# Optimization experiments

Hardware: AMD Instinct MI355X
Metric: run time of the kernel (lower is better)

The kernel has to match this reference:

```python
import jax, jax.numpy as jnp
import numpy as np

N_WAY = 5
K_SHOT = 1
PROJ_DIM = 64
TEMPERATURE = 0.2
EPS_COS = 1e-12   # F.normalize eps in InnerproductSimilarity (cosine)
EPS_L2 = 1e-16    # _l2norm eps


def setup_inputs() -> dict:
    key = jax.random.key(0)
    ks = jax.random.split(key, 8)
    b, q, u, c, h, w = 2, 15, 20, 64, 21, 21
    s = N_WAY * K_SHOT
    std = float(np.sqrt(2.0 / PROJ_DIM))  # kaiming init used for 1x1 conv heads
    return {
        "support_xf": jax.random.normal(ks[0], (b, s, c, h, w), jnp.float32),
        "support_y": jax.random.randint(ks[1], (b, s), 0, N_WAY),
        "query_xf": jax.random.normal(ks[2], (b, q, c, h, w), jnp.float32),
        "query_y": jax.random.randint(ks[3], (b, q), 0, N_WAY),
        "unlabeled_xf": jax.random.normal(ks[4], (b, u, c, h, w), jnp.float32),
        "key_w": jax.random.normal(ks[5], (PROJ_DIM, c), jnp.float32) * std,
        "query_w": jax.random.normal(ks[6], (PROJ_DIM, c), jnp.float32) * std,
        "value_w": jax.random.normal(ks[7], (PROJ_DIM, c), jnp.float32) * std,
    }


def _dual_nn_selection(support_xf, unlabeled_xf):
    """Mutual-NN (dual NN) selection of unlabeled positions per class.
    Returns padded gather indices idx [b,n_way,L], 0/1 validity sel [b,n_way,L], and L.
    L is data-dependent (max per-(batch,class) count), computed eagerly like the
    original torch code's umask_length."""
    b, u, c, h, w = unlabeled_xf.shape
    M_u, M_s = u * h * w, K_SHOT * h * w
    unl = jnp.transpose(unlabeled_xf, (0, 2, 1, 3, 4)).reshape(b, c, M_u)  # [b,c,M_u]
    sup = jnp.transpose(support_xf.reshape(b, N_WAY, K_SHOT, c, h, w), (0, 1, 3, 2, 4, 5)).reshape(b, N_WAY, c, M_s)
    # cosine InnerproductSimilarity: normalize over channel dim
    sup_n = sup / jnp.maximum(jnp.linalg.norm(sup, axis=2, keepdims=True), EPS_COS)
    unl_n = unl / jnp.maximum(jnp.linalg.norm(unl, axis=1, keepdims=True), EPS_COS)
    u2s = jnp.einsum('bcm,bncs->bnms', unl_n, sup_n)  # [b,n_way,M_u,M_s]
    flat = jnp.transpose(u2s, (0, 2, 1, 3)).reshape(b, M_u, N_WAY * M_s)
    s_near = jnp.argmax(flat, axis=1)   # [b, n_way*M_s] nearest unlabeled pos per support slot
    u_near = jnp.argmax(flat, axis=2)   # [b, M_u] nearest support slot per unlabeled pos
    mutual = (jnp.take_along_axis(s_near, u_near, axis=1) == jnp.arange(M_u)[None, :])  # [b,M_u]
    cls = jnp.argmax(jnp.max(u2s, axis=-1), axis=1)  # [b,M_u] class assignment
    umask = jnp.transpose(jax.nn.one_hot(cls, N_WAY, dtype=jnp.float32), (0, 2, 1)) \
            * mutual[:, None, :].astype(jnp.float32)  # [b,n_way,M_u]
    L = int(jnp.max(jnp.sum(umask, axis=-1)))  # umask_length (data-dependent)
    order = jnp.argsort(-umask, axis=-1)       # stable: selected positions first, original order
    idx = order[:, :, :L]                      # [b,n_way,L]
    sel = jnp.take_along_axis(umask, idx, axis=-1)  # 1 = real feature, 0 = zero padding
    return idx, sel, L


def _forward_core(support_xf, query_xf, unlabeled_xf, key_w, query_w, value_w, query_y, idx, sel):
    b, q, c, h, w = query_xf.shape
    hw = h * w
    u = unlabeled_xf.shape[1]
    M_u, M_s = u * hw, K_SHOT * hw
    unl = jnp.transpose(unlabeled_xf, (0, 2, 1, 3, 4)).reshape(b, c, M_u)
    sup = jnp.transpose(support_xf.reshape(b, N_WAY, K_SHOT, c, h, w), (0, 1, 3, 2, 4, 5)).reshape(b, N_WAY, c, M_s)
    # ragged per-class scatter realized as padded gather (zeros where sel==0)
    gathered = jnp.take_along_axis(unl[:, None, :, :], idx[:, :, None, :], axis=-1)  # [b,n_way,c,L]
    unl_dual = gathered * sel[:, :, None, :]
    s_cat_u = jnp.concatenate([sup, unl_dual], axis=-1)  # [b,n_way,c,M_s+L]
    # 1x1 conv heads == channel matmuls
    qf = query_xf.reshape(b, q, c, hw)
    q_proj = jnp.einsum('oc,bqcm->bqom', query_w, qf)   # [b,q,64,hw]
    v_query = jnp.einsum('oc,bqcm->bqom', value_w, qf)  # [b,q,64,hw]
    k_sup = jnp.einsum('oc,bncl->bnol', key_w, s_cat_u)
    v_sup = jnp.einsum('oc,bncl->bnol', value_w, s_cat_u)
    simi = jnp.einsum('bqom,bnol->bqnml', q_proj, k_sup) / np.float32(np.sqrt(PROJ_DIM))  # [b,q,n,hw,Ms+L]
    Lt = simi.shape[-1]
    # _MNN with compensate_for_single == False (encoder == 'FourLayer_64F')
    merged = jnp.transpose(simi, (0, 1, 3, 2, 4)).reshape(b, q, hw, N_WAY * Lt)
    q_near = jnp.argmax(merged, axis=-1)  # [b,q,hw]
    s_near = jnp.argmax(merged, axis=-2)  # [b,q,n_way*Lt]
    q_mask = (jnp.take_along_axis(s_near, q_near, axis=-1) == jnp.arange(hw)[None, None, :]).astype(simi.dtype)
    att = jax.nn.softmax(simi * q_mask[:, :, None, :, None], axis=-1)
    aligned = jnp.einsum('bqnml,bnol->bqnmo', att, v_sup)  # [b,q,n_way,hw,64]
    aligned = aligned / (jnp.linalg.norm(aligned, axis=-1, keepdims=True) + EPS_L2)
    vq = v_query / (jnp.linalg.norm(v_query, axis=2, keepdims=True) + EPS_L2)
    simi2 = (jnp.einsum('bqnmo,bqok->bqnmk', aligned, vq) + 1.0) * 0.5  # FourLayer_64F rescale
    logits = jnp.sum(jnp.max(simi2, axis=-2), axis=-1).reshape(b * q, N_WAY)  # topk(1,-2)+mean == max
    logp = jax.nn.log_softmax(logits / np.float32(TEMPERATURE), axis=-1)
    y = query_y.reshape(b * q)
    return -jnp.mean(jnp.take_along_axis(logp, y[:, None], axis=1))  # CrossEntropyLoss


def reference(support_xf, support_y, query_xf, query_y, unlabeled_xf, key_w, query_w, value_w):
    idx, sel, _ = _dual_nn_selection(support_xf, unlabeled_xf)
    return _forward_core(support_xf, query_xf, unlabeled_xf, key_w, query_w, value_w, query_y, idx, sel)
```

## Files before the change

kernel.cpp:

```cpp
#include <hip/hip_runtime.h>
#include <math.h>

#define B 2
#define Q 15
#define U 20
#define C 64
#define HW 441
#define NW 5
#define MU (U*HW)
#define MS HW
#define NJ (NW*MS)
#define PD 64
#define LCAP NJ
#define LTCAP 896
#define SCAP 896
#define MSP 448
#define MUP 8832
#define NJP 2304
#define NEGF (-3.402823466e38f)

__device__ unsigned long long g_snearpack[B*NJ];
__device__ unsigned long long g_unearpack[B*MU];
__device__ int   g_counts[B*NW];
__device__ int   g_L[1];
__device__ int   g_selidx[B*NW*LCAP];
__device__ float g_unln[(size_t)B*C*MUP];
__device__ float g_supn[(size_t)B*C*NJP];
__device__ float g_ksup[(size_t)B*NW*PD*LTCAP];
__device__ float g_vsup[(size_t)B*NW*PD*LTCAP];
__device__ float g_vsupT[(size_t)B*NW*LTCAP*PD];
__device__ float g_vbarn[B*NW*PD];
__device__ float g_qproj[(size_t)B*Q*PD*MSP];
__device__ float g_vqn[(size_t)B*Q*PD*MSP];
__device__ unsigned long long g_rowpack[(size_t)B*Q*NW*MSP];
__device__ unsigned long long g_snear2pack[(size_t)B*Q*NW*LTCAP];
__device__ int   g_qmrows[B*Q*MSP];
__device__ int   g_qmcount[B*Q];
__device__ unsigned g_cmax[(size_t)B*Q*NW*MSP];
__device__ float g_logits[B*Q*NW];
__device__ float g_scores[(size_t)B*Q*NW*MSP*SCAP];

__device__ __forceinline__ unsigned enc_f(float f){
  unsigned b=__float_as_uint(f);
  return (b&0x80000000u)? ~b : (b|0x80000000u);
}
__device__ __forceinline__ float dec_f(unsigned k){
  unsigned b=(k&0x80000000u)?(k^0x80000000u):~k;
  return __uint_as_float(b);
}
__device__ __forceinline__ unsigned long long pk_make(float v,int idx){
  return ((unsigned long long)enc_f(v)<<32)|(unsigned)~(unsigned)idx;
}
__device__ __forceinline__ int pk_idx(unsigned long long p){
  return (int)~(unsigned)(p&0xFFFFFFFFull);
}

__global__ void k_init(){
  int i=blockIdx.x*256+threadIdx.x;
  if (i<B*NJ) g_snearpack[i]=0ull;
  if (i<B*MU) g_unearpack[i]=0ull;
  if (i<B*Q*NW*MSP){ g_rowpack[i]=0ull; g_cmax[i]=0u; }
  if (i<B*Q*NW*LTCAP) g_snear2pack[i]=0ull;
  if (i<B*C*(MUP-MU)){
    int b=i/(C*(MUP-MU)), r=i%(C*(MUP-MU)), c=r/(MUP-MU), m=MU+r%(MUP-MU);
    g_unln[((size_t)b*C+c)*MUP+m]=0.f;
  }
  if (i<B*C*(NJP-NJ)){
    int b=i/(C*(NJP-NJ)), r=i%(C*(NJP-NJ)), c=r/(NJP-NJ), j=NJ+r%(NJP-NJ);
    g_supn[((size_t)b*C+c)*NJP+j]=0.f;
  }
  if (i==0) g_L[0]=0;
}

__global__ void k_norms(const float* __restrict__ sup, const float* __restrict__ unl){
  int i=blockIdx.x*256+threadIdx.x;
  if (i<B*MU){
    int b=i/MU, m=i%MU, ui=m/HW, p=m%HW;
    const float* base=unl+((size_t)(b*U+ui)*C)*HW+p;
    float ss=0.f;
    for (int c=0;c<C;c++){ float x=base[(size_t)c*HW]; ss+=x*x; }
    float rn=1.f/fmaxf(sqrtf(ss),1e-12f);
    for (int c=0;c<C;c++) g_unln[((size_t)b*C+c)*MUP+m]=base[(size_t)c*HW]*rn;
  }
  if (i<B*NJ){
    int b=i/NJ, j=i%NJ, n=j/MS, s=j%MS;
    const float* base=sup+((size_t)(b*NW+n)*C)*HW+s;
    float ss=0.f;
    for (int c=0;c<C;c++){ float x=base[(size_t)c*HW]; ss+=x*x; }
    float rn=1.f/fmaxf(sqrtf(ss),1e-12f);
    for (int c=0;c<C;c++) g_supn[((size_t)b*C+c)*NJP+j]=base[(size_t)c*HW]*rn;
  }
}

__global__ __launch_bounds__(256) void k_u2s(){
  int blk=blockIdx.x;
  int jc=blk%18; blk/=18;
  int rb=blk%69; int b=blk/69;
  int m0=rb*128, j0=jc*128;
  int mv=min(128,MU-m0);
  int jv=min(128,NJ-j0);
  int tid=threadIdx.x, tm=tid>>4, tl=tid&15;
  int lane=tid&63, w=tid>>6;
  __shared__ __align__(16) float Ut[32*128];
  __shared__ __align__(16) float Pt[32*128];
  __shared__ unsigned long long colred[512];
  const size_t ub=(size_t)b*C*MUP+m0;
  const size_t pb=(size_t)b*C*NJP+j0;
  float s[8][8]={};
  #pragma unroll
  for (int h=0;h<2;h++){
    __syncthreads();
    for (int k4=tid;k4<1024;k4+=256){
      int c=k4>>5, mq=k4&31;
      *(float4*)&Ut[c*128+mq*4]=*(const float4*)&g_unln[ub+(size_t)(h*32+c)*MUP+mq*4];
      *(float4*)&Pt[c*128+mq*4]=*(const float4*)&g_supn[pb+(size_t)(h*32+c)*NJP+mq*4];
    }
    __syncthreads();
    for (int c=0;c<32;c++){
      float a[8],b0[4],b1[4];
      *(float4*)&a[0]=*(const float4*)&Ut[c*128+tm*8];
      *(float4*)&a[4]=*(const float4*)&Ut[c*128+tm*8+4];
      *(float4*)b0=*(const float4*)&Pt[c*128+tl*4];
      *(float4*)b1=*(const float4*)&Pt[c*128+64+tl*4];
      #pragma unroll
      for (int i=0;i<8;i++)
        #pragma unroll
        for (int j=0;j<4;j++){ s[i][j]=fmaf(a[i],b0[j],s[i][j]); s[i][j+4]=fmaf(a[i],b1[j],s[i][j+4]); }
    }
  }
  #pragma unroll
  for (int i=0;i<8;i++){
    int mm=tm*8+i;
    unsigned long long p=0ull;
    if (mm<mv){
      #pragma unroll
      for (int j=0;j<8;j++){
        int jj=(j<4)?(tl*4+j):(64+tl*4+(j-4));
        if (jj<jv){
          unsigned long long c2=pk_make(s[i][j],j0+jj);
          if (c2>p) p=c2;
        }
      }
    }
    #pragma unroll
    for (int mk=1;mk<16;mk<<=1){ unsigned long long o=__shfl_xor(p,mk); if (o>p) p=o; }
    if (tl==0 && mm<mv && p) atomicMax(&g_unearpack[b*MU+m0+mm],p);
  }
  #pragma unroll
  for (int j=0;j<8;j++){
    int jj=(j<4)?(tl*4+j):(64+tl*4+(j-4));
    unsigned long long p=0ull;
    #pragma unroll
    for (int i=0;i<8;i++){
      int mm=tm*8+i;
      if (mm<mv){
        unsigned long long c2=pk_make(s[i][j],m0+mm);
        if (c2>p) p=c2;
      }
    }
    {
      unsigned long long o=__shfl_xor(p,16); if (o>p) p=o;
      o=__shfl_xor(p,32); if (o>p) p=o;
    }
    if ((lane>>4)==0) colred[w*128+jj]=p;
  }
  __syncthreads();
  if (tid<128 && tid<jv){
    unsigned long long p=colred[tid];
    if (colred[128+tid]>p) p=colred[128+tid];
    if (colred[256+tid]>p) p=colred[256+tid];
    if (colred[384+tid]>p) p=colred[384+tid];
    if (p) atomicMax(&g_snearpack[b*NJ+j0+tid],p);
  }
}

__global__ __launch_bounds__(256) void k_compact(){
  int b=blockIdx.x/NW, n=blockIdx.x%NW;
  int tid=threadIdx.x, lane=tid&63, w=tid>>6;
  __shared__ int wtot[4];
  int base=0;
  for (int m0=0;m0<MU;m0+=256){
    int m=m0+tid;
    bool flag=false;
    if (m<MU){
      int j=pk_idx(g_unearpack[b*MU+m]);
      flag=(j/MS==n) && (pk_idx(g_snearpack[b*NJ+j])==m);
    }
    unsigned long long bal=__ballot(flag);
    if (lane==0) wtot[w]=(int)__popcll(bal);
    __syncthreads();
    int wpre=0, tot=0;
    #pragma unroll
    for (int ww=0;ww<4;ww++){ if (ww<w) wpre+=wtot[ww]; tot+=wtot[ww]; }
    if (flag){
      int pre=(int)__popcll(bal&((1ull<<lane)-1ull));
      g_selidx[(b*NW+n)*LCAP+base+wpre+pre]=m;
    }
    base+=tot;
    __syncthreads();
  }
  if (tid==0){ g_counts[b*NW+n]=base; atomicMax(&g_L[0],base); }
}

__global__ __launch_bounds__(256) void k_kv(const float* __restrict__ sup, const float* __restrict__ unl,
                                            const float* __restrict__ kw, const float* __restrict__ vw){
  int blk=blockIdx.x;
  int lb=blk%(LTCAP/64); blk/=(LTCAP/64);
  int n=blk%NW, b=blk/NW;
  int Lt=MS+g_L[0];
  if (lb*64>=Lt) return;
  int cnt=g_counts[b*NW+n];
  int tid=threadIdx.x, lane=tid&63, w=tid>>6;
  __shared__ float F[4096];
  __shared__ const float* ptr_s[64];
  if (tid<64){
    int l=lb*64+tid;
    const float* p=nullptr;
    if (l<MS) p=&sup[((size_t)(b*NW+n)*C)*HW+l];
    else if (l<MS+cnt){
      int mg=g_selidx[(b*NW+n)*LCAP+(l-MS)];
      int ui=mg/HW, pp=mg%HW;
      p=&unl[((size_t)(b*U+ui)*C)*HW+pp];
    }
    ptr_s[tid]=p;
  }
  __syncthreads();
  for (int k=tid;k<4096;k+=256){
    int c=k>>6, ll=k&63;
    const float* p=ptr_s[ll];
    F[c*64+ll]=p?p[(size_t)c*HW]:0.f;
  }
  __syncthreads();
  int l=lb*64+lane;
  size_t ob=((size_t)(b*NW+n)*PD)*LTCAP+l;
  size_t tb=((size_t)(b*NW+n)*LTCAP+l)*PD;
  for (int oo=0;oo<16;oo++){
    int o=w*16+oo;
    float ka=0.f, va=0.f;
    for (int c=0;c<C;c++){ float f=F[c*64+lane]; ka=fmaf(kw[o*C+c],f,ka); va=fmaf(vw[o*C+c],f,va); }
    g_ksup[ob+(size_t)o*LTCAP]=ka;
    g_vsup[ob+(size_t)o*LTCAP]=va;
    g_vsupT[tb+o]=va;
  }
}

__global__ __launch_bounds__(256) void k_vbar(){
  int bn=blockIdx.x;
  int tid=threadIdx.x, lane=tid&63, w=tid>>6;
  int cnt=g_counts[bn];
  int Lt=MS+g_L[0];
  __shared__ float vb_s[64];
  for (int oo=0;oo<16;oo++){
    int o=w*16+oo;
    const float* row=&g_vsup[((size_t)bn*PD+o)*LTCAP];
    float s=0.f;
    for (int l=lane;l<MS+cnt;l+=64) s+=row[l];
    #pragma unroll
    for (int mk=1;mk<64;mk<<=1) s+=__shfl_xor(s,mk);
    if (lane==0) vb_s[o]=s/(float)Lt;
  }
  __syncthreads();
  if (tid<64){
    float v=vb_s[tid];
    float ss=v*v;
    #pragma unroll
    for (int mk=1;mk<64;mk<<=1) ss+=__shfl_xor(ss,mk);
    g_vbarn[bn*PD+tid]=v/(sqrtf(ss)+1e-16f);
  }
}

__global__ __launch_bounds__(256) void k_qproj(const float* __restrict__ qx, const float* __restrict__ qw,
                                               const float* __restrict__ vw){
  int blk=blockIdx.x;
  int mt=blk%7; blk/=7;
  int bq=blk;
  int tid=threadIdx.x, lane=tid&63, w=tid>>6;
  __shared__ float F[4096];
  __shared__ float ssp[256];
  for (int k=tid;k<4096;k+=256){
    int c=k>>6, mm=k&63, m=mt*64+mm;
    F[c*64+mm]=(m<MS)?qx[((size_t)bq*C+c)*HW+m]:0.f;
  }
  __syncthreads();
  int m=mt*64+lane;
  size_t ob=(size_t)bq*PD*MSP+m;
  float va[16]; float ssl=0.f;
  for (int oo=0;oo<16;oo++){
    int o=w*16+oo;
    float qa=0.f, v=0.f;
    for (int c=0;c<C;c++){ float f=F[c*64+lane]; qa=fmaf(qw[o*C+c],f,qa); v=fmaf(vw[o*C+c],f,v); }
    g_qproj[ob+(size_t)o*MSP]=qa;
    va[oo]=v; ssl=fmaf(v,v,ssl);
  }
  ssp[tid]=ssl;
  __syncthreads();
  float ss=ssp[lane]+ssp[64+lane]+ssp[128+lane]+ssp[192+lane];
  float rn=1.f/(sqrtf(ss)+1e-16f);
  for (int oo=0;oo<16;oo++) g_vqn[ob+(size_t)(w*16+oo)*MSP]=va[oo]*rn;
}

__global__ __launch_bounds__(256) void k_passA(){
  int blk=blockIdx.x;
  int lc=blk%7; blk/=7;
  int mh=blk%4; blk/=4;
  int n=blk%NW; blk/=NW;
  int bq=blk; int b=bq/Q;
  int Lt=MS+g_L[0];
  int nch=(Lt+127)>>7;
  if (lc>=nch) return;
  int l0=lc<<7, lv=min(128,Lt-l0);
  int tid=threadIdx.x, tm=tid>>4, tl=tid&15;
  int lane=tid&63, w=tid>>6;
  int bqn=bq*NW+n;
  int m0=mh*128;
  __shared__ __align__(16) float Qt[32*128];
  __shared__ __align__(16) float Kt[32*128];
  __shared__ unsigned long long colred[512];
  const size_t qb=(size_t)bq*PD*MSP;
  const size_t kb=(size_t)(b*NW+n)*PD*LTCAP;
  float s[8][8]={};
  #pragma unroll
  for (int h=0;h<2;h++){
    __syncthreads();
    for (int k4=tid;k4<1024;k4+=256){
      int o=k4>>5, mq=k4&31;
      int m=m0+mq*4;
      float4 v=make_float4(0.f,0.f,0.f,0.f);
      if (m<MSP) v=*(const float4*)&g_qproj[qb+(size_t)(h*32+o)*MSP+m];
      *(float4*)&Qt[o*128+mq*4]=v;
      *(float4*)&Kt[o*128+mq*4]=*(const float4*)&g_ksup[kb+(size_t)(h*32+o)*LTCAP+l0+mq*4];
    }
    __syncthreads();
    for (int c=0;c<32;c++){
      float a[8],b0[4],b1[4];
      *(float4*)&a[0]=*(const float4*)&Qt[c*128+tm*8];
      *(float4*)&a[4]=*(const float4*)&Qt[c*128+tm*8+4];
      *(float4*)b0=*(const float4*)&Kt[c*128+tl*4];
      *(float4*)b1=*(const float4*)&Kt[c*128+64+tl*4];
      #pragma unroll
      for (int i=0;i<8;i++)
        #pragma unroll
        for (int j=0;j<4;j++){ s[i][j]=fmaf(a[i],b0[j],s[i][j]); s[i][j+4]=fmaf(a[i],b1[j],s[i][j+4]); }
    }
  }
  #pragma unroll
  for (int i=0;i<8;i++)
    #pragma unroll
    for (int j=0;j<8;j++) s[i][j]*=0.125f;
  #pragma unroll
  for (int i=0;i<8;i++){
    int m=m0+tm*8+i;
    if (m<MS){
      size_t sbase=((size_t)bqn*MSP+m)*SCAP+l0;
      *(float4*)&g_scores[sbase+tl*4]   =make_float4(s[i][0],s[i][1],s[i][2],s[i][3]);
      *(float4*)&g_scores[sbase+64+tl*4]=make_float4(s[i][4],s[i][5],s[i][6],s[i][7]);
    }
  }
  #pragma unroll
  for (int i=0;i<8;i++){
    int m=m0+tm*8+i;
    unsigned long long p=0ull;
    if (m<MS){
      #pragma unroll
      for (int j=0;j<8;j++){
        int jj=(j<4)?(tl*4+j):(64+tl*4+(j-4));
        if (jj<lv){
          unsigned long long c2=pk_make(s[i][j],l0+jj);
          if (c2>p) p=c2;
        }
      }
    }
    #pragma unroll
    for (int mk=1;mk<16;mk<<=1){ unsigned long long o=__shfl_xor(p,mk); if (o>p) p=o; }
    if (tl==0 && m<MS && p) atomicMax(&g_rowpack[(size_t)bqn*MSP+m],p);
  }
  #pragma unroll
  for (int j=0;j<8;j++){
    int jj=(j<4)?(tl*4+j):(64+tl*4+(j-4));
    unsigned long long p=0ull;
    #pragma unroll
    for (int i=0;i<8;i++){
      int m=m0+tm*8+i;
      if (m<MS){
        unsigned long long c2=pk_make(s[i][j],m);
        if (c2>p) p=c2;
      }
    }
    {
      unsigned long long o=__shfl_xor(p,16); if (o>p) p=o;
      o=__shfl_xor(p,32); if (o>p) p=o;
    }
    if ((lane>>4)==0) colred[w*128+jj]=p;
  }
  __syncthreads();
  if (tid<128 && tid<lv){
    unsigned long long p=colred[tid];
    if (colred[128+tid]>p) p=colred[128+tid];
    if (colred[256+tid]>p) p=colred[256+tid];
    if (colred[384+tid]>p) p=colred[384+tid];
    if (p) atomicMax(&g_snear2pack[(size_t)bqn*LTCAP+l0+tid],p);
  }
}

__global__ __launch_bounds__(256) void k_qmask(){
  int bq=blockIdx.x;
  int tid=threadIdx.x, lane=tid&63, w=tid>>6;
  __shared__ int wtot[4];
  int base=0;
  for (int m0=0;m0<MS;m0+=256){
    int m=m0+tid;
    bool qm=false;
    if (m<MS){
      unsigned bhv=0u; unsigned long long bp=0ull; int bn=0;
      #pragma unroll
      for (int n=0;n<NW;n++){
        unsigned long long pk=g_rowpack[(size_t)(bq*NW+n)*MSP+m];
        unsigned hv=(unsigned)(pk>>32);
        if (hv>bhv){bhv=hv;bp=pk;bn=n;}
      }
      int bl=pk_idx(bp);
      qm=(pk_idx(g_snear2pack[(size_t)(bq*NW+bn)*LTCAP+bl])==m);
    }
    unsigned long long bal=__ballot(qm);
    if (lane==0) wtot[w]=(int)__popcll(bal);
    __syncthreads();
    int wpre=0, tot=0;
    #pragma unroll
    for (int ww=0;ww<4;ww++){ if (ww<w) wpre+=wtot[ww]; tot+=wtot[ww]; }
    if (qm){
      int pre=(int)__popcll(bal&((1ull<<lane)-1ull));
      g_qmrows[bq*MSP+base+wpre+pre]=m;
    }
    base+=tot;
    __syncthreads();
  }
  if (tid==0) g_qmcount[bq]=base;
}

#define EXPROW(i, svi) { \
    float e0=(tl*4+0<lv)?__expf((svi).x-rmax[i]):0.f; \
    float e1=(tl*4+1<lv)?__expf((svi).y-rmax[i]):0.f; \
    float e2=(tl*4+2<lv)?__expf((svi).z-rmax[i]):0.f; \
    float e3=(tl*4+3<lv)?__expf((svi).w-rmax[i]):0.f; \
    lsum[i]+=(e0+e1)+(e2+e3); \
    *(float4*)&Pt[(tm*4+(i))*68+tl*4]=make_float4(e0,e1,e2,e3); }
#define KPLOAD(kp, it, ktv) { int kk=tid+(it)*256; int o=kk>>4, kq=kk&15; \
    kp=*(const float4*)&g_vqn[qb+(size_t)o*MSP+(ktv)*64+kq*4]; }
#define KPSTORE(kp, it) { int kk=tid+(it)*256; int o=kk>>4, kq=kk&15; \
    *(float4*)&Vt[o*64+kq*4]=kp; }
__global__ __launch_bounds__(256,4) void k_passB(){
  int blk=blockIdx.x;
  int rt=blk%7; blk/=7;
  int n=blk%NW; blk/=NW;
  int bq=blk; int b=bq/Q;
  int nm=g_qmcount[bq];
  if (rt*64>=nm) return;
  int bqn=bq*NW+n;
  int Lt=MS+g_L[0];
  int nch=(Lt+63)>>6;
  int tid=threadIdx.x, tm=tid>>4, tl=tid&15;
  __shared__ __align__(16) float Vt[4096];
  __shared__ __align__(16) float Pt[64*68];
  __shared__ int rows_s[64];
  if (tid<64){ int g=rt*64+tid; rows_s[tid]=(g<nm)?g_qmrows[bq*MSP+g]:0; }
  __syncthreads();
  float rmax[4]; size_t sb[4];
  #pragma unroll
  for (int i=0;i<4;i++){
    int row=rows_s[tm*4+i];
    rmax[i]=dec_f((unsigned)(g_rowpack[(size_t)bqn*MSP+row]>>32));
    sb[i]=((size_t)bqn*MSP+row)*SCAP;
  }
  const size_t vb=(size_t)(b*NW+n)*LTCAP*PD;
  const size_t qb=(size_t)bq*PD*MSP;
  float lsum[4]={0.f,0.f,0.f,0.f};
  float acc[4][4]={};
  float4 sv0,sv1,sv2,sv3, vp0,vp1,vp2,vp3;
  sv0=*(const float4*)&g_scores[sb[0]+tl*4];
  sv1=*(const float4*)&g_scores[sb[1]+tl*4];
  sv2=*(const float4*)&g_scores[sb[2]+tl*4];
  sv3=*(const float4*)&g_scores[sb[3]+tl*4];
  {
    const float* src=&g_vsupT[vb];
    vp0=*(const float4*)&src[(tid     )*4];
    vp1=*(const float4*)&src[(tid+256 )*4];
    vp2=*(const float4*)&src[(tid+512 )*4];
    vp3=*(const float4*)&src[(tid+768 )*4];
  }
  for (int lc=0;lc<nch;lc++){
    int l0=lc<<6, lv=min(64,Lt-l0);
    __syncthreads();
    *(float4*)&Vt[(tid     )*4]=vp0;
    *(float4*)&Vt[(tid+256 )*4]=vp1;
    *(float4*)&Vt[(tid+512 )*4]=vp2;
    *(float4*)&Vt[(tid+768 )*4]=vp3;
    EXPROW(0,sv0) EXPROW(1,sv1) EXPROW(2,sv2) EXPROW(3,sv3)
    __syncthreads();
    if (lc+1<nch){
      int l1=(lc+1)<<6;
      sv0=*(const float4*)&g_scores[sb[0]+l1+tl*4];
      sv1=*(const float4*)&g_scores[sb[1]+l1+tl*4];
      sv2=*(const float4*)&g_scores[sb[2]+l1+tl*4];
      sv3=*(const float4*)&g_scores[sb[3]+l1+tl*4];
      const float* src=&g_vsupT[vb+(size_t)l1*PD];
      vp0=*(const float4*)&src[(tid     )*4];
      vp1=*(const float4*)&src[(tid+256 )*4];
      vp2=*(const float4*)&src[(tid+512 )*4];
      vp3=*(const float4*)&src[(tid+768 )*4];
    }
    for (int l4=0;l4<64;l4+=4){
      float4 pq[4];
      #pragma unroll
      for (int i=0;i<4;i++) pq[i]=*(const float4*)&Pt[(tm*4+i)*68+l4];
      #pragma unroll
      for (int u=0;u<4;u++){
        float4 v4=*(const float4*)&Vt[(l4+u)*64+tl*4];
        #pragma unroll
        for (int i=0;i<4;i++){
          float p=((const float*)&pq[i])[u];
          acc[i][0]=fmaf(p,v4.x,acc[i][0]);
          acc[i][1]=fmaf(p,v4.y,acc[i][1]);
          acc[i][2]=fmaf(p,v4.z,acc[i][2]);
          acc[i][3]=fmaf(p,v4.w,acc[i][3]);
        }
      }
    }
  }
  float4 kp0,kp1,kp2,kp3;
  KPLOAD(kp0,0,0) KPLOAD(kp1,1,0) KPLOAD(kp2,2,0) KPLOAD(kp3,3,0)
  float rn[4];
  #pragma unroll
  for (int i=0;i<4;i++){
    float ls=lsum[i];
    #pragma unroll
    for (int mk=1;mk<16;mk<<=1) ls+=__shfl_xor(ls,mk);
    float ss=0.f;
    #pragma unroll
    for (int j=0;j<4;j++){ acc[i][j]/=ls; ss=fmaf(acc[i][j],acc[i][j],ss); }
    #pragma unroll
    for (int mk=1;mk<16;mk<<=1) ss+=__shfl_xor(ss,mk);
    rn[i]=1.f/(sqrtf(ss)+1e-16f);
  }
  __syncthreads();
  #pragma unroll
  for (int i=0;i<4;i++)
    *(float4*)&Pt[(tm*4+i)*68+tl*4]=make_float4(acc[i][0],acc[i][1],acc[i][2],acc[i][3]);
  int rowok[4];
  #pragma unroll
  for (int i=0;i<4;i++) rowok[i]=(rt*64+tm*4+i<nm);
  for (int kt=0;kt<7;kt++){
    __syncthreads();
    KPSTORE(kp0,0) KPSTORE(kp1,1) KPSTORE(kp2,2) KPSTORE(kp3,3)
    __syncthreads();
    if (kt+1<7){
      KPLOAD(kp0,0,kt+1) KPLOAD(kp1,1,kt+1) KPLOAD(kp2,2,kt+1) KPLOAD(kp3,3,kt+1)
    }
    float d[4][4]={};
    for (int o=0;o<64;o++){
      float a[4], bv4[4];
      #pragma unroll
      for (int i=0;i<4;i++) a[i]=Pt[(tm*4+i)*68+o];
      *(float4*)bv4=*(const float4*)&Vt[o*64+tl*4];
      #pragma unroll
      for (int i=0;i<4;i++)
        #pragma unroll
        for (int j=0;j<4;j++) d[i][j]=fmaf(a[i],bv4[j],d[i][j]);
    }
    #pragma unroll
    for (int j=0;j<4;j++){
      int kg=kt*64+tl*4+j;
      float mv=NEGF;
      #pragma unroll
      for (int i=0;i<4;i++) if (rowok[i]) mv=fmaxf(mv,d[i][j]*rn[i]);
      mv=fmaxf(mv,__shfl_xor(mv,16));
      mv=fmaxf(mv,__shfl_xor(mv,32));
      if (((tid>>4)&3)==0 && kg<MS && mv>-1e37f)
        atomicMax(&g_cmax[(size_t)bqn*MSP+kg],enc_f(mv));
    }
  }
}

__global__ __launch_bounds__(256) void k_logits(){
  int bqn=blockIdx.x;
  int n=bqn%NW, bq=bqn/NW, b=bq/Q;
  int tid=threadIdx.x;
  int nm=g_qmcount[bq];
  __shared__ float red[256];
  __shared__ float vb_s[64];
  if (tid<64) vb_s[tid]=g_vbarn[(b*NW+n)*PD+tid];
  __syncthreads();
  const float* vq=&g_vqn[(size_t)bq*PD*MSP];
  float p=0.f;
  for (int k=tid;k<MS;k+=256){
    float v=dec_f(g_cmax[(size_t)bqn*MSP+k]);
    if (nm<MS){
      float d=0.f;
      for (int o=0;o<PD;o++) d=fmaf(vb_s[o],vq[(size_t)o*MSP+k],d);
      v=fmaxf(v,d);
    }
    p+=(v+1.f)*0.5f;
  }
  red[tid]=p; __syncthreads();
  for (int s=128;s;s>>=1){ if (tid<s) red[tid]+=red[tid+s]; __syncthreads(); }
  if (tid==0) g_logits[bqn]=red[0];
}

__global__ void k_loss(const int* __restrict__ qy, float* __restrict__ out){
  int t=threadIdx.x;
  float lp=0.f;
  if (t<B*Q){
    int y=qy[t];
    float xv[NW]; float mxv=NEGF;
    #pragma unroll
    for (int n=0;n<NW;n++){ xv[n]=g_logits[t*NW+n]*5.f; mxv=fmaxf(mxv,xv[n]); }
    float s=0.f, xy=0.f;
    #pragma unroll
    for (int n=0;n<NW;n++){ s+=__expf(xv[n]-mxv); if (n==y) xy=xv[n]; }
    lp=xy-mxv-logf(s);
  }
  #pragma unroll
  for (int off=32;off;off>>=1) lp+=__shfl_down(lp,off);
  if (t==0) out[0]=-lp/(float)(B*Q);
}

extern "C" void kernel_launch(void* const* d_in, const int* in_sizes, int n_in,
                              void* d_out, int out_size, void* d_ws, size_t ws_size,
                              hipStream_t stream) {
  (void)in_sizes; (void)n_in; (void)out_size; (void)d_ws; (void)ws_size;
  const float* sup=(const float*)d_in[0];
  const float* qx =(const float*)d_in[2];
  const int*   qy =(const int*)d_in[3];
  const float* unl=(const float*)d_in[4];
  const float* kw =(const float*)d_in[5];
  const float* qw =(const float*)d_in[6];
  const float* vw =(const float*)d_in[7];
  float* out=(float*)d_out;

  k_init   <<<525,256,0,stream>>>();
  k_norms  <<<69,256,0,stream>>>(sup,unl);
  k_u2s    <<<B*69*18,256,0,stream>>>();
  k_compact<<<B*NW,256,0,stream>>>();
  k_kv     <<<B*NW*(LTCAP/64),256,0,stream>>>(sup,unl,kw,vw);
  k_vbar   <<<B*NW,256,0,stream>>>();
  k_qproj  <<<B*Q*7,256,0,stream>>>(qx,qw,vw);
  k_passA  <<<B*Q*NW*28,256,0,stream>>>();
  k_qmask  <<<B*Q,256,0,stream>>>();
  k_passB  <<<B*Q*NW*7,256,0,stream>>>();
  k_logits <<<B*Q*NW,256,0,stream>>>();
  k_loss   <<<1,64,0,stream>>>(qy,out);
}
```

Measured before the change: 652.3 us.

## Split passB into split-L PV, finalize, and tiled simi2 kernels

The fused passB kernel is split into three launches. The first splits the softmax-times-V accumulation over the key dimension into two halves and writes partial sums. The second combines the halves and normalizes the rows. The third computes the aligned-query similarity max with one block per key tile instead of looping over seven tiles. This exposes more blocks, which should help occupancy on a large GPU, at the cost of extra global round-trips for the partial accumulators and two additional kernel launches.

```diff
diff --git a/kernel.cpp b/kernel.cpp
--- a/kernel.cpp
+++ b/kernel.cpp
@@ -12,6 +12,7 @@
 #define NJ (NW*MS)
 #define PD 64
 #define LCAP NJ
+#define BQN (B*Q*NW)
 #define LTCAP 896
 #define SCAP 896
 #define MSP 448
@@ -39,6 +40,10 @@
 __device__ unsigned g_cmax[(size_t)B*Q*NW*MSP];
 __device__ float g_logits[B*Q*NW];
 __device__ float g_scores[(size_t)B*Q*NW*MSP*SCAP];
+__device__ float g_accp[(size_t)2*BQN*MSP*PD];
+__device__ float g_lsump[2*BQN*MSP];
+__device__ float g_aligned[(size_t)BQN*MSP*PD];
+__device__ float g_rnrow[BQN*MSP];
 
 __device__ __forceinline__ unsigned enc_f(float f){
   unsigned b=__float_as_uint(f);
@@ -444,12 +449,9 @@
     float e3=(tl*4+3<lv)?__expf((svi).w-rmax[i]):0.f; \
     lsum[i]+=(e0+e1)+(e2+e3); \
     *(float4*)&Pt[(tm*4+(i))*68+tl*4]=make_float4(e0,e1,e2,e3); }
-#define KPLOAD(kp, it, ktv) { int kk=tid+(it)*256; int o=kk>>4, kq=kk&15; \
-    kp=*(const float4*)&g_vqn[qb+(size_t)o*MSP+(ktv)*64+kq*4]; }
-#define KPSTORE(kp, it) { int kk=tid+(it)*256; int o=kk>>4, kq=kk&15; \
-    *(float4*)&Vt[o*64+kq*4]=kp; }
-__global__ __launch_bounds__(256,4) void k_passB(){
+__global__ __launch_bounds__(256,4) void k_pv(){
   int blk=blockIdx.x;
+  int lh=blk&1; blk>>=1;
   int rt=blk%7; blk/=7;
   int n=blk%NW; blk/=NW;
   int bq=blk; int b=bq/Q;
@@ -458,6 +460,7 @@
   int bqn=bq*NW+n;
   int Lt=MS+g_L[0];
   int nch=(Lt+63)>>6;
+  int c0=lh*7, c1=min(nch,c0+7);
   int tid=threadIdx.x, tm=tid>>4, tl=tid&15;
   __shared__ __align__(16) float Vt[4096];
   __shared__ __align__(16) float Pt[64*68];
@@ -472,111 +475,151 @@
     sb[i]=((size_t)bqn*MSP+row)*SCAP;
   }
   const size_t vb=(size_t)(b*NW+n)*LTCAP*PD;
-  const size_t qb=(size_t)bq*PD*MSP;
   float lsum[4]={0.f,0.f,0.f,0.f};
   float acc[4][4]={};
-  float4 sv0,sv1,sv2,sv3, vp0,vp1,vp2,vp3;
-  sv0=*(const float4*)&g_scores[sb[0]+tl*4];
-  sv1=*(const float4*)&g_scores[sb[1]+tl*4];
-  sv2=*(const float4*)&g_scores[sb[2]+tl*4];
-  sv3=*(const float4*)&g_scores[sb[3]+tl*4];
-  {
-    const float* src=&g_vsupT[vb];
-    vp0=*(const float4*)&src[(tid     )*4];
-    vp1=*(const float4*)&src[(tid+256 )*4];
-    vp2=*(const float4*)&src[(tid+512 )*4];
-    vp3=*(const float4*)&src[(tid+768 )*4];
-  }
-  for (int lc=0;lc<nch;lc++){
-    int l0=lc<<6, lv=min(64,Lt-l0);
-    __syncthreads();
-    *(float4*)&Vt[(tid     )*4]=vp0;
-    *(float4*)&Vt[(tid+256 )*4]=vp1;
-    *(float4*)&Vt[(tid+512 )*4]=vp2;
-    *(float4*)&Vt[(tid+768 )*4]=vp3;
-    EXPROW(0,sv0) EXPROW(1,sv1) EXPROW(2,sv2) EXPROW(3,sv3)
-    __syncthreads();
-    if (lc+1<nch){
-      int l1=(lc+1)<<6;
-      sv0=*(const float4*)&g_scores[sb[0]+l1+tl*4];
-      sv1=*(const float4*)&g_scores[sb[1]+l1+tl*4];
-      sv2=*(const float4*)&g_scores[sb[2]+l1+tl*4];
-      sv3=*(const float4*)&g_scores[sb[3]+l1+tl*4];
-      const float* src=&g_vsupT[vb+(size_t)l1*PD];
+  if (c0<c1){
+    float4 sv0,sv1,sv2,sv3, vp0,vp1,vp2,vp3;
+    {
+      int l0=c0<<6;
+      sv0=*(const float4*)&g_scores[sb[0]+l0+tl*4];
+      sv1=*(const float4*)&g_scores[sb[1]+l0+tl*4];
+      sv2=*(const float4*)&g_scores[sb[2]+l0+tl*4];
+      sv3=*(const float4*)&g_scores[sb[3]+l0+tl*4];
+      const float* src=&g_vsupT[vb+(size_t)l0*PD];
       vp0=*(const float4*)&src[(tid     )*4];
       vp1=*(const float4*)&src[(tid+256 )*4];
       vp2=*(const float4*)&src[(tid+512 )*4];
       vp3=*(const float4*)&src[(tid+768 )*4];
     }
-    for (int l4=0;l4<64;l4+=4){
-      float4 pq[4];
-      #pragma unroll
-      for (int i=0;i<4;i++) pq[i]=*(const float4*)&Pt[(tm*4+i)*68+l4];
-      #pragma unroll
-      for (int u=0;u<4;u++){
-        float4 v4=*(const float4*)&Vt[(l4+u)*64+tl*4];
+    for (int lc=c0;lc<c1;lc++){
+      int l0=lc<<6, lv=min(64,Lt-l0);
+      __syncthreads();
+      *(float4*)&Vt[(tid     )*4]=vp0;
+      *(float4*)&Vt[(tid+256 )*4]=vp1;
+      *(float4*)&Vt[(tid+512 )*4]=vp2;
+      *(float4*)&Vt[(tid+768 )*4]=vp3;
+      EXPROW(0,sv0) EXPROW(1,sv1) EXPROW(2,sv2) EXPROW(3,sv3)
+      __syncthreads();
+      if (lc+1<c1){
+        int l1=(lc+1)<<6;
+        sv0=*(const float4*)&g_scores[sb[0]+l1+tl*4];
+        sv1=*(const float4*)&g_scores[sb[1]+l1+tl*4];
+        sv2=*(const float4*)&g_scores[sb[2]+l1+tl*4];
+        sv3=*(const float4*)&g_scores[sb[3]+l1+tl*4];
+        const float* src=&g_vsupT[vb+(size_t)l1*PD];
+        vp0=*(const float4*)&src[(tid     )*4];
+        vp1=*(const float4*)&src[(tid+256 )*4];
+        vp2=*(const float4*)&src[(tid+512 )*4];
+        vp3=*(const float4*)&src[(tid+768 )*4];
+      }
+      for (int l4=0;l4<64;l4+=4){
+        float4 pq[4];
         #pragma unroll
-        for (int i=0;i<4;i++){
-          float p=((const float*)&pq[i])[u];
-          acc[i][0]=fmaf(p,v4.x,acc[i][0]);
-          acc[i][1]=fmaf(p,v4.y,acc[i][1]);
-          acc[i][2]=fmaf(p,v4.z,acc[i][2]);
-          acc[i][3]=fmaf(p,v4.w,acc[i][3]);
+        for (int i=0;i<4;i++) pq[i]=*(const float4*)&Pt[(tm*4+i)*68+l4];
+        #pragma unroll
+        for (int u=0;u<4;u++){
+          float4 v4=*(const float4*)&Vt[(l4+u)*64+tl*4];
+          #pragma unroll
+          for (int i=0;i<4;i++){
+            float p=((const float*)&pq[i])[u];
+            acc[i][0]=fmaf(p,v4.x,acc[i][0]);
+            acc[i][1]=fmaf(p,v4.y,acc[i][1]);
+            acc[i][2]=fmaf(p,v4.z,acc[i][2]);
+            acc[i][3]=fmaf(p,v4.w,acc[i][3]);
+          }
         }
       }
     }
   }
-  float4 kp0,kp1,kp2,kp3;
-  KPLOAD(kp0,0,0) KPLOAD(kp1,1,0) KPLOAD(kp2,2,0) KPLOAD(kp3,3,0)
-  float rn[4];
+  const size_t lbase=((size_t)lh*BQN+bqn)*MSP;
   #pragma unroll
   for (int i=0;i<4;i++){
     float ls=lsum[i];
     #pragma unroll
     for (int mk=1;mk<16;mk<<=1) ls+=__shfl_xor(ls,mk);
+    int g=rt*64+tm*4+i;
+    if (tl==0) g_lsump[lbase+g]=ls;
+    *(float4*)&g_accp[(lbase+g)*PD+tl*4]=make_float4(acc[i][0],acc[i][1],acc[i][2],acc[i][3]);
+  }
+}
+
+__global__ __launch_bounds__(256) void k_fin(){
+  int blk=blockIdx.x;
+  int rt=blk%7; blk/=7;
+  int n=blk%NW; blk/=NW;
+  int bq=blk;
+  int nm=g_qmcount[bq];
+  if (rt*64>=nm) return;
+  int bqn=bq*NW+n;
+  int tid=threadIdx.x, tm=tid>>4, tl=tid&15;
+  #pragma unroll
+  for (int i=0;i<4;i++){
+    int g=rt*64+tm*4+i;
+    size_t r0=(size_t)bqn*MSP+g;
+    size_t r1=(size_t)(BQN+bqn)*MSP+g;
+    float4 a0=*(const float4*)&g_accp[r0*PD+tl*4];
+    float4 a1=*(const float4*)&g_accp[r1*PD+tl*4];
+    float ls=g_lsump[r0]+g_lsump[r1];
+    float a[4]={a0.x+a1.x, a0.y+a1.y, a0.z+a1.z, a0.w+a1.w};
     float ss=0.f;
     #pragma unroll
-    for (int j=0;j<4;j++){ acc[i][j]/=ls; ss=fmaf(acc[i][j],acc[i][j],ss); }
+    for (int j=0;j<4;j++){ a[j]/=ls; ss=fmaf(a[j],a[j],ss); }
     #pragma unroll
     for (int mk=1;mk<16;mk<<=1) ss+=__shfl_xor(ss,mk);
-    rn[i]=1.f/(sqrtf(ss)+1e-16f);
-  }
-  __syncthreads();
-  #pragma unroll
-  for (int i=0;i<4;i++)
-    *(float4*)&Pt[(tm*4+i)*68+tl*4]=make_float4(acc[i][0],acc[i][1],acc[i][2],acc[i][3]);
-  int rowok[4];
-  #pragma unroll
-  for (int i=0;i<4;i++) rowok[i]=(rt*64+tm*4+i<nm);
-  for (int kt=0;kt<7;kt++){
-    __syncthreads();
-    KPSTORE(kp0,0) KPSTORE(kp1,1) KPSTORE(kp2,2) KPSTORE(kp3,3)
-    __syncthreads();
-    if (kt+1<7){
-      KPLOAD(kp0,0,kt+1) KPLOAD(kp1,1,kt+1) KPLOAD(kp2,2,kt+1) KPLOAD(kp3,3,kt+1)
-    }
-    float d[4][4]={};
-    for (int o=0;o<64;o++){
-      float a[4], bv4[4];
+    float rn=1.f/(sqrtf(ss)+1e-16f);
+    *(float4*)&g_aligned[r0*PD+tl*4]=make_float4(a[0],a[1],a[2],a[3]);
+    if (tl==0) g_rnrow[r0]=rn;
+  }
+}
+
+__global__ __launch_bounds__(256) void k_simi2(){
+  int blk=blockIdx.x;
+  int kt=blk%7; blk/=7;
+  int rt=blk%7; blk/=7;
+  int n=blk%NW; blk/=NW;
+  int bq=blk;
+  int nm=g_qmcount[bq];
+  if (rt*64>=nm) return;
+  int bqn=bq*NW+n;
+  int tid=threadIdx.x, tm=tid>>4, tl=tid&15;
+  __shared__ __align__(16) float Vt[4096];
+  __shared__ __align__(16) float Pt[64*68];
+  __shared__ float rn_s[64];
+  const size_t qb=(size_t)bq*PD*MSP;
+  for (int k=tid;k<1024;k+=256){
+    int r=k>>4, oq=k&15;
+    *(float4*)&Pt[r*68+oq*4]=*(const float4*)&g_aligned[((size_t)bqn*MSP+rt*64+r)*PD+oq*4];
+  }
+  if (tid<64) rn_s[tid]=g_rnrow[(size_t)bqn*MSP+rt*64+tid];
+  for (int k=tid;k<1024;k+=256){
+    int o=k>>4, kq=k&15;
+    *(float4*)&Vt[o*64+kq*4]=*(const float4*)&g_vqn[qb+(size_t)o*MSP+kt*64+kq*4];
+  }
+  __syncthreads();
+  float d[4][4]={};
+  for (int o=0;o<64;o++){
+    float a[4], bv4[4];
+    #pragma unroll
+    for (int i=0;i<4;i++) a[i]=Pt[(tm*4+i)*68+o];
+    *(float4*)bv4=*(const float4*)&Vt[o*64+tl*4];
+    #pragma unroll
+    for (int i=0;i<4;i++)
       #pragma unroll
-      for (int i=0;i<4;i++) a[i]=Pt[(tm*4+i)*68+o];
-      *(float4*)bv4=*(const float4*)&Vt[o*64+tl*4];
-      #pragma unroll
-      for (int i=0;i<4;i++)
-        #pragma unroll
-        for (int j=0;j<4;j++) d[i][j]=fmaf(a[i],bv4[j],d[i][j]);
-    }
-    #pragma unroll
-    for (int j=0;j<4;j++){
-      int kg=kt*64+tl*4+j;
-      float mv=NEGF;
-      #pragma unroll
-      for (int i=0;i<4;i++) if (rowok[i]) mv=fmaxf(mv,d[i][j]*rn[i]);
-      mv=fmaxf(mv,__shfl_xor(mv,16));
-      mv=fmaxf(mv,__shfl_xor(mv,32));
-      if (((tid>>4)&3)==0 && kg<MS && mv>-1e37f)
-        atomicMax(&g_cmax[(size_t)bqn*MSP+kg],enc_f(mv));
-    }
+      for (int j=0;j<4;j++) d[i][j]=fmaf(a[i],bv4[j],d[i][j]);
+  }
+  int rowok[4]; float rn[4];
+  #pragma unroll
+  for (int i=0;i<4;i++){ rowok[i]=(rt*64+tm*4+i<nm); rn[i]=rn_s[tm*4+i]; }
+  #pragma unroll
+  for (int j=0;j<4;j++){
+    int kg=kt*64+tl*4+j;
+    float mv=NEGF;
+    #pragma unroll
+    for (int i=0;i<4;i++) if (rowok[i]) mv=fmaxf(mv,d[i][j]*rn[i]);
+    mv=fmaxf(mv,__shfl_xor(mv,16));
+    mv=fmaxf(mv,__shfl_xor(mv,32));
+    if (((tid>>4)&3)==0 && kg<MS && mv>-1e37f)
+      atomicMax(&g_cmax[(size_t)bqn*MSP+kg],enc_f(mv));
   }
 }
 
@@ -645,7 +688,9 @@
   k_qproj  <<<B*Q*7,256,0,stream>>>(qx,qw,vw);
   k_passA  <<<B*Q*NW*28,256,0,stream>>>();
   k_qmask  <<<B*Q,256,0,stream>>>();
-  k_passB  <<<B*Q*NW*7,256,0,stream>>>();
+  k_pv     <<<B*Q*NW*7*2,256,0,stream>>>();
+  k_fin    <<<B*Q*NW*7,256,0,stream>>>();
+  k_simi2  <<<B*Q*NW*7*7,256,0,stream>>>();
   k_logits <<<B*Q*NW,256,0,stream>>>();
   k_loss   <<<1,64,0,stream>>>(qy,out);
 }
```

After: 769.5 us. +18.0%, slower.
